# Optimization experiments

Measured on AMD Instinct MI355X. Metric: run time of the kernel, lower is better.

The kernel has to match this reference:

```python
import jax, jax.numpy as jnp
import numpy as np

N_NODES = 50000
IN_CH = 128
OUT_CH = 64
N_EDGES = 800000


def setup_inputs() -> dict:
    key = jax.random.key(0)
    k_x, k_e, k_w, k_b = jax.random.split(key, 4)
    x = jax.random.normal(k_x, (N_NODES, IN_CH), dtype=jnp.float32)
    edge_index = jax.random.randint(k_e, (2, N_EDGES), 0, N_NODES, dtype=jnp.int64)
    # nn.Linear(in, out, bias=False): weight [out, in], applied as x @ W^T
    W = jax.random.normal(k_w, (OUT_CH, IN_CH), dtype=jnp.float32) * (1.0 / np.sqrt(IN_CH))
    bias = jax.random.normal(k_b, (OUT_CH,), dtype=jnp.float32) * 0.02
    return {"x": x, "edge_index": edge_index, "W": W, "bias": bias}


def reference(x, edge_index, W, bias):
    # linear projection (no bias): [N, in] @ [in, out] -> [N, out]
    h = x @ W.T
    src = edge_index[0]
    dst = edge_index[1]
    # gather source node feats per edge: [E, out]
    msgs = h[src]
    # scatter_add into dest nodes: [N, out]
    out = jax.ops.segment_sum(msgs, dst, num_segments=h.shape[0])
    return out + bias
```

## Files before the change

### kernel.cpp

```cpp
#include <hip/hip_runtime.h>

#define IN_CH 128
#define OUT_CH 64
#define TN 64
#define XS_STRIDE 132
#define WS_STRIDE 129

#define PBLOCKS 512
#define NB 800
#define CAPA 8
#define DCAP 32

__device__ __forceinline__ unsigned f2bf(float f) {
    unsigned u = __float_as_uint(f);
    return (u + 0x7FFFu + ((u >> 16) & 1u)) >> 16;
}

__device__ __forceinline__ void fma4(float4& acc, float s, const float4& wv) {
    acc.x += s * wv.x;
    acc.y += s * wv.y;
    acc.z += s * wv.z;
    acc.w += s * wv.w;
}

__global__ __launch_bounds__(256) void k_fusedA(const float* __restrict__ x,
                                                const float* __restrict__ W,
                                                unsigned* __restrict__ h16,
                                                const int* __restrict__ ei,
                                                unsigned* __restrict__ cells,
                                                int* __restrict__ cntA,
                                                uint2* __restrict__ spill,
                                                int* __restrict__ spillCount,
                                                int nNodes, int nEdges, int gemmBlocks) {
    __shared__ float smem[TN * XS_STRIDE + IN_CH * OUT_CH];
    __shared__ int is64s;
    int tid = threadIdx.x;

    if (blockIdx.x >= gemmBlocks) {
        unsigned* lists = (unsigned*)smem;
        int* curs = (int*)smem + NB * CAPA;
        int pblk = blockIdx.x - gemmBlocks;
        for (int i = tid; i < NB; i += 256) curs[i] = 0;
        if (tid == 0) {
            int v = 1;
#pragma unroll
            for (int j = 0; j < 16; ++j)
                if (ei[2 * j + 1] != 0) v = 0;
            is64s = v;
        }
        __syncthreads();
        int is64 = is64s;

        int chunk = (nEdges + PBLOCKS - 1) / PBLOCKS;
        int e0 = pblk * chunk;
        int e1 = min(e0 + chunk, nEdges);
        for (int e = e0 + tid; e < e1; e += 256) {
            int src, dst;
            if (is64) {
                src = ((const int2*)ei)[e].x;
                dst = ((const int2*)ei)[nEdges + e].x;
            } else {
                src = ei[e];
                dst = ei[nEdges + e];
            }
            if ((unsigned)src >= (unsigned)nNodes) src = 0;
            if ((unsigned)dst >= (unsigned)nNodes) dst = 0;
            int bucket = dst >> 6;
            int rank = (bucket < NB) ? atomicAdd(&curs[bucket], 1) : CAPA;
            if (rank < CAPA) {
                lists[bucket * CAPA + rank] = (unsigned)src | ((unsigned)(dst & 63) << 16);
            } else {
                int sp = atomicAdd(spillCount, 1);
                if (sp < nEdges) spill[sp] = make_uint2((unsigned)src, (unsigned)dst);
            }
        }
        __syncthreads();

        size_t base = (size_t)pblk * NB;
        uint4* cells4 = (uint4*)(cells + base * CAPA);
        for (int j = tid; j < NB * CAPA / 4; j += 256)
            cells4[j] = *(const uint4*)(lists + 4 * j);
        for (int i = tid; i < NB; i += 256)
            cntA[base + i] = min(curs[i], CAPA);
        return;
    }

    float* u  = smem;
    float* wt = smem + TN * XS_STRIDE;
    int nodeBase = blockIdx.x * TN;

    {
        const float4* W4 = (const float4*)W;
        for (int i = tid; i < IN_CH * OUT_CH / 4; i += 256) {
            float4 v = W4[i];
            int o = i >> 5;
            int k = (i & 31) * 4;
            float* d = u + o * WS_STRIDE + k;
            d[0] = v.x; d[1] = v.y; d[2] = v.z; d[3] = v.w;
        }
    }
    __syncthreads();
    {
        int o = tid & 63;
        int k0 = (tid >> 6) * 32;
#pragma unroll 8
        for (int k = k0; k < k0 + 32; ++k)
            wt[k * OUT_CH + o] = u[o * WS_STRIDE + k];
    }
    __syncthreads();
    {
        int remRows = nNodes - nodeBase;
        if (remRows > TN) remRows = TN;
        const float4* X4 = (const float4*)(x + (size_t)nodeBase * IN_CH);
        for (int i = tid; i < TN * IN_CH / 4; i += 256) {
            int r = i >> 5;
            int k = (i & 31) * 4;
            float4 v = make_float4(0.f, 0.f, 0.f, 0.f);
            if (r < remRows) v = X4[i];
            *(float4*)(u + r * XS_STRIDE + k) = v;
        }
    }
    __syncthreads();

    int tx = tid & 15;
    int ty = tid >> 4;

    float4 acc[4];
#pragma unroll
    for (int i = 0; i < 4; ++i) acc[i] = make_float4(0.f, 0.f, 0.f, 0.f);

    const float* wcol = wt + tx * 4;
#pragma unroll 4
    for (int k = 0; k < IN_CH; k += 4) {
        float4 w0 = *(const float4*)(wcol + (k + 0) * OUT_CH);
        float4 w1 = *(const float4*)(wcol + (k + 1) * OUT_CH);
        float4 w2 = *(const float4*)(wcol + (k + 2) * OUT_CH);
        float4 w3 = *(const float4*)(wcol + (k + 3) * OUT_CH);
#pragma unroll
        for (int i = 0; i < 4; ++i) {
            float4 a = *(const float4*)(u + (ty * 4 + i) * XS_STRIDE + k);
            fma4(acc[i], a.x, w0);
            fma4(acc[i], a.y, w1);
            fma4(acc[i], a.z, w2);
            fma4(acc[i], a.w, w3);
        }
    }

#pragma unroll
    for (int i = 0; i < 4; ++i) {
        int n = nodeBase + ty * 4 + i;
        if (n < nNodes) {
            uint2 pk;
            pk.x = f2bf(acc[i].x) | (f2bf(acc[i].y) << 16);
            pk.y = f2bf(acc[i].z) | (f2bf(acc[i].w) << 16);
            *(uint2*)(h16 + (size_t)n * 32 + tx * 2) = pk;
        }
    }
}

__global__ __launch_bounds__(1024) void k_fusedB(const unsigned* __restrict__ cells,
                                                 const int* __restrict__ cntA,
                                                 const unsigned* __restrict__ h16,
                                                 const float* __restrict__ bias,
                                                 float* __restrict__ out,
                                                 uint2* __restrict__ spill,
                                                 int* __restrict__ spillCount,
                                                 int nNodes, int nEdges) {
    __shared__ unsigned nl[64 * DCAP];
    __shared__ int nc[64];
    int tid = threadIdx.x;
    int b = blockIdx.x;
    int nodeBase = b * 64;

    if (tid < 64) nc[tid] = 0;
    __syncthreads();

    if (b < NB) {
        for (int blk = tid; blk < PBLOCKS; blk += 1024) {
            int c = cntA[(size_t)blk * NB + b];
            const unsigned* cb = cells + ((size_t)blk * NB + b) * CAPA;
            uint4 w0 = *(const uint4*)(cb + 0);
            uint4 w1 = *(const uint4*)(cb + 4);
            unsigned w[CAPA] = {w0.x, w0.y, w0.z, w0.w, w1.x, w1.y, w1.z, w1.w};
#pragma unroll
            for (int r = 0; r < CAPA; ++r) {
                if (r < c) {
                    unsigned rec = w[r];
                    int sub = (int)(rec >> 16);
                    int rank = atomicAdd(&nc[sub], 1);
                    if (rank < DCAP) {
                        nl[sub * DCAP + rank] = rec & 0xFFFFu;
                    } else {
                        int sp = atomicAdd(spillCount, 1);
                        if (sp < nEdges) spill[sp] = make_uint2(rec & 0xFFFFu, (unsigned)(nodeBase + sub));
                    }
                }
            }
        }
    }
    __syncthreads();

    int lane = tid & 63;
    int wv   = tid >> 6;
    int half = lane >> 5;
    int cp   = lane & 31;
    float2 bv = *(const float2*)(bias + cp * 2);

#pragma unroll
    for (int i = 0; i < 4; ++i) {
        int sub = wv * 4 + i;
        int node = nodeBase + sub;
        if (node >= nNodes) continue;

        int d = nc[sub];
        if (d > DCAP) d = DCAP;
        int jend = (d + 1) & ~1;

        int myslot = (lane < d) ? (int)nl[sub * DCAP + lane] : 0;

        float2 acc = {0.f, 0.f};
        int j = half;
        for (; j + 6 < jend; j += 8) {
            int s0 = __shfl(myslot, j, 64);
            int s1 = __shfl(myslot, j + 2, 64);
            int s2 = __shfl(myslot, j + 4, 64);
            int s3 = __shfl(myslot, j + 6, 64);
            unsigned v0 = h16[(size_t)s0 * 32 + cp];
            unsigned v1 = h16[(size_t)s1 * 32 + cp];
            unsigned v2 = h16[(size_t)s2 * 32 + cp];
            unsigned v3 = h16[(size_t)s3 * 32 + cp];
            if (j + 6 >= d) v3 = 0;
            acc.x += __uint_as_float(v0 << 16);
            acc.y += __uint_as_float(v0 & 0xFFFF0000u);
            acc.x += __uint_as_float(v1 << 16);
            acc.y += __uint_as_float(v1 & 0xFFFF0000u);
            acc.x += __uint_as_float(v2 << 16);
            acc.y += __uint_as_float(v2 & 0xFFFF0000u);
            acc.x += __uint_as_float(v3 << 16);
            acc.y += __uint_as_float(v3 & 0xFFFF0000u);
        }
        for (; j < jend; j += 2) {
            int s = __shfl(myslot, j, 64);
            unsigned v = h16[(size_t)s * 32 + cp];
            if (j >= d) v = 0;
            acc.x += __uint_as_float(v << 16);
            acc.y += __uint_as_float(v & 0xFFFF0000u);
        }

        acc.x += __shfl_down(acc.x, 32, 64);
        acc.y += __shfl_down(acc.y, 32, 64);
        if (half == 0) {
            float2 o;
            o.x = acc.x + bv.x;
            o.y = acc.y + bv.y;
            *(float2*)(out + (size_t)node * OUT_CH + cp * 2) = o;
        }
    }
}

__global__ __launch_bounds__(256) void k_spill(const uint2* __restrict__ spill,
                                               const int* __restrict__ spillCount,
                                               const unsigned* __restrict__ h16,
                                               float* __restrict__ out, int nEdges) {
    int n = *spillCount;
    if (n > nEdges) n = nEdges;
    long long total = (long long)n * 32;
    for (long long t = blockIdx.x * 256 + threadIdx.x; t < total; t += (long long)gridDim.x * 256) {
        int e = (int)(t >> 5);
        int cp = (int)(t & 31);
        uint2 sd = spill[e];
        unsigned v = h16[(size_t)sd.x * 32 + cp];
        float* o = out + (size_t)sd.y * OUT_CH + cp * 2;
        unsafeAtomicAdd(o + 0, __uint_as_float(v << 16));
        unsafeAtomicAdd(o + 1, __uint_as_float(v & 0xFFFF0000u));
    }
}

extern "C" void kernel_launch(void* const* d_in, const int* in_sizes, int n_in,
                              void* d_out, int out_size, void* d_ws, size_t ws_size,
                              hipStream_t stream) {
    const float* x    = (const float*)d_in[0];
    const int*   ei   = (const int*)d_in[1];
    const float* W    = (const float*)d_in[2];
    const float* bias = (const float*)d_in[3];
    float* out = (float*)d_out;

    int nNodes = in_sizes[0] / IN_CH;
    int nEdges = in_sizes[1] / 2;
    int gemmBlocks = (nNodes + TN - 1) / TN;
    int realBuckets = (nNodes + 63) / 64;

    char* p = (char*)d_ws;
    auto alloc = [&](size_t bytes) {
        char* r = p;
        p += (bytes + 255) & ~(size_t)255;
        return r;
    };
    unsigned* h16        = (unsigned*)alloc((size_t)nNodes * 32 * sizeof(unsigned));
    unsigned* cells      = (unsigned*)alloc((size_t)PBLOCKS * NB * CAPA * sizeof(unsigned));
    int*      cntA       = (int*)alloc((size_t)PBLOCKS * NB * sizeof(int));
    uint2*    spill      = (uint2*)alloc((size_t)nEdges * sizeof(uint2));
    int*      spillCount = (int*)alloc(sizeof(int));

    hipMemsetAsync(spillCount, 0, sizeof(int), stream);
    k_fusedA<<<gemmBlocks + PBLOCKS, 256, 0, stream>>>(x, W, h16, ei, cells, cntA,
                                                       spill, spillCount, nNodes, nEdges, gemmBlocks);
    k_fusedB<<<realBuckets, 1024, 0, stream>>>(cells, cntA, h16, bias, out,
                                               spill, spillCount, nNodes, nEdges);
    k_spill<<<64, 256, 0, stream>>>(spill, spillCount, h16, out, nEdges);
}
```

Measured before the change: 138.3 us.

## Pack bucket counts into cell records and interleave partition and GEMM blocks

Removes the separate per-cell count array by storing each cell's count in the top 4 bits of its first record, so the consumer kernel gets the count from the same 32-byte load and skips one scattered read per cell. It also spreads the edge-partition blocks evenly among the GEMM blocks in the grid instead of putting them all at the end, so memory-bound and compute-bound work run on the GPU at the same time. The packing relies on source indices fitting in 16 bits and the count fitting in 4 bits. The consumer now masks the sub-bucket field to 6 bits so the packed count does not corrupt the first record.

```diff
diff --git a/kernel.cpp b/kernel.cpp
--- a/kernel.cpp
+++ b/kernel.cpp
@@ -28,19 +28,22 @@
                                                 unsigned* __restrict__ h16,
                                                 const int* __restrict__ ei,
                                                 unsigned* __restrict__ cells,
-                                                int* __restrict__ cntA,
                                                 uint2* __restrict__ spill,
                                                 int* __restrict__ spillCount,
-                                                int nNodes, int nEdges, int gemmBlocks) {
+                                                int nNodes, int nEdges, int totalBlocks) {
     __shared__ float smem[TN * XS_STRIDE + IN_CH * OUT_CH];
     __shared__ int is64s;
     int tid = threadIdx.x;
 
-    if (blockIdx.x >= gemmBlocks) {
+    int i = blockIdx.x;
+    long long t = (long long)i * PBLOCKS;
+    int pid = (int)(t / totalBlocks);
+    int isPartA = (int)((t + PBLOCKS) / totalBlocks) > pid;
+
+    if (isPartA) {
         unsigned* lists = (unsigned*)smem;
         int* curs = (int*)smem + NB * CAPA;
-        int pblk = blockIdx.x - gemmBlocks;
-        for (int i = tid; i < NB; i += 256) curs[i] = 0;
+        for (int k = tid; k < NB; k += 256) curs[k] = 0;
         if (tid == 0) {
             int v = 1;
 #pragma unroll
@@ -52,7 +55,7 @@
         int is64 = is64s;
 
         int chunk = (nEdges + PBLOCKS - 1) / PBLOCKS;
-        int e0 = pblk * chunk;
+        int e0 = pid * chunk;
         int e1 = min(e0 + chunk, nEdges);
         for (int e = e0 + tid; e < e1; e += 256) {
             int src, dst;
@@ -76,25 +79,30 @@
         }
         __syncthreads();
 
-        size_t base = (size_t)pblk * NB;
+        size_t base = (size_t)pid * NB;
         uint4* cells4 = (uint4*)(cells + base * CAPA);
-        for (int j = tid; j < NB * CAPA / 4; j += 256)
-            cells4[j] = *(const uint4*)(lists + 4 * j);
-        for (int i = tid; i < NB; i += 256)
-            cntA[base + i] = min(curs[i], CAPA);
+        for (int j = tid; j < NB * CAPA / 4; j += 256) {
+            uint4 v = *(const uint4*)(lists + 4 * j);
+            if ((j & 1) == 0) {
+                int cell = j >> 1;
+                v.x = (v.x & 0x0FFFFFFFu) | ((unsigned)min(curs[cell], CAPA) << 28);
+            }
+            cells4[j] = v;
+        }
         return;
     }
 
+    int gid = i - pid;
     float* u  = smem;
     float* wt = smem + TN * XS_STRIDE;
-    int nodeBase = blockIdx.x * TN;
+    int nodeBase = gid * TN;
 
     {
         const float4* W4 = (const float4*)W;
-        for (int i = tid; i < IN_CH * OUT_CH / 4; i += 256) {
-            float4 v = W4[i];
-            int o = i >> 5;
-            int k = (i & 31) * 4;
+        for (int j = tid; j < IN_CH * OUT_CH / 4; j += 256) {
+            float4 v = W4[j];
+            int o = j >> 5;
+            int k = (j & 31) * 4;
             float* d = u + o * WS_STRIDE + k;
             d[0] = v.x; d[1] = v.y; d[2] = v.z; d[3] = v.w;
         }
@@ -112,11 +120,11 @@
         int remRows = nNodes - nodeBase;
         if (remRows > TN) remRows = TN;
         const float4* X4 = (const float4*)(x + (size_t)nodeBase * IN_CH);
-        for (int i = tid; i < TN * IN_CH / 4; i += 256) {
-            int r = i >> 5;
-            int k = (i & 31) * 4;
+        for (int j = tid; j < TN * IN_CH / 4; j += 256) {
+            int r = j >> 5;
+            int k = (j & 31) * 4;
             float4 v = make_float4(0.f, 0.f, 0.f, 0.f);
-            if (r < remRows) v = X4[i];
+            if (r < remRows) v = X4[j];
             *(float4*)(u + r * XS_STRIDE + k) = v;
         }
     }
@@ -127,7 +135,7 @@
 
     float4 acc[4];
 #pragma unroll
-    for (int i = 0; i < 4; ++i) acc[i] = make_float4(0.f, 0.f, 0.f, 0.f);
+    for (int q = 0; q < 4; ++q) acc[q] = make_float4(0.f, 0.f, 0.f, 0.f);
 
     const float* wcol = wt + tx * 4;
 #pragma unroll 4
@@ -137,29 +145,28 @@
         float4 w2 = *(const float4*)(wcol + (k + 2) * OUT_CH);
         float4 w3 = *(const float4*)(wcol + (k + 3) * OUT_CH);
 #pragma unroll
-        for (int i = 0; i < 4; ++i) {
-            float4 a = *(const float4*)(u + (ty * 4 + i) * XS_STRIDE + k);
-            fma4(acc[i], a.x, w0);
-            fma4(acc[i], a.y, w1);
-            fma4(acc[i], a.z, w2);
-            fma4(acc[i], a.w, w3);
-        }
-    }
-
-#pragma unroll
-    for (int i = 0; i < 4; ++i) {
-        int n = nodeBase + ty * 4 + i;
+        for (int q = 0; q < 4; ++q) {
+            float4 a = *(const float4*)(u + (ty * 4 + q) * XS_STRIDE + k);
+            fma4(acc[q], a.x, w0);
+            fma4(acc[q], a.y, w1);
+            fma4(acc[q], a.z, w2);
+            fma4(acc[q], a.w, w3);
+        }
+    }
+
+#pragma unroll
+    for (int q = 0; q < 4; ++q) {
+        int n = nodeBase + ty * 4 + q;
         if (n < nNodes) {
             uint2 pk;
-            pk.x = f2bf(acc[i].x) | (f2bf(acc[i].y) << 16);
-            pk.y = f2bf(acc[i].z) | (f2bf(acc[i].w) << 16);
+            pk.x = f2bf(acc[q].x) | (f2bf(acc[q].y) << 16);
+            pk.y = f2bf(acc[q].z) | (f2bf(acc[q].w) << 16);
             *(uint2*)(h16 + (size_t)n * 32 + tx * 2) = pk;
         }
     }
 }
 
 __global__ __launch_bounds__(1024) void k_fusedB(const unsigned* __restrict__ cells,
-                                                 const int* __restrict__ cntA,
                                                  const unsigned* __restrict__ h16,
                                                  const float* __restrict__ bias,
                                                  float* __restrict__ out,
@@ -177,16 +184,17 @@
 
     if (b < NB) {
         for (int blk = tid; blk < PBLOCKS; blk += 1024) {
-            int c = cntA[(size_t)blk * NB + b];
             const unsigned* cb = cells + ((size_t)blk * NB + b) * CAPA;
             uint4 w0 = *(const uint4*)(cb + 0);
             uint4 w1 = *(const uint4*)(cb + 4);
+            int c = (int)(w0.x >> 28);
+            if (c > CAPA) c = CAPA;
             unsigned w[CAPA] = {w0.x, w0.y, w0.z, w0.w, w1.x, w1.y, w1.z, w1.w};
 #pragma unroll
             for (int r = 0; r < CAPA; ++r) {
                 if (r < c) {
                     unsigned rec = w[r];
-                    int sub = (int)(rec >> 16);
+                    int sub = (int)(rec >> 16) & 63;
                     int rank = atomicAdd(&nc[sub], 1);
                     if (rank < DCAP) {
                         nl[sub * DCAP + rank] = rec & 0xFFFFu;
@@ -207,8 +215,8 @@
     float2 bv = *(const float2*)(bias + cp * 2);
 
 #pragma unroll
-    for (int i = 0; i < 4; ++i) {
-        int sub = wv * 4 + i;
+    for (int q = 0; q < 4; ++q) {
+        int sub = wv * 4 + q;
         int node = nodeBase + sub;
         if (node >= nNodes) continue;
 
@@ -289,6 +297,7 @@
     int nEdges = in_sizes[1] / 2;
     int gemmBlocks = (nNodes + TN - 1) / TN;
     int realBuckets = (nNodes + 63) / 64;
+    int totalBlocks = gemmBlocks + PBLOCKS;
 
     char* p = (char*)d_ws;
     auto alloc = [&](size_t bytes) {
@@ -298,14 +307,13 @@
     };
     unsigned* h16        = (unsigned*)alloc((size_t)nNodes * 32 * sizeof(unsigned));
     unsigned* cells      = (unsigned*)alloc((size_t)PBLOCKS * NB * CAPA * sizeof(unsigned));
-    int*      cntA       = (int*)alloc((size_t)PBLOCKS * NB * sizeof(int));
     uint2*    spill      = (uint2*)alloc((size_t)nEdges * sizeof(uint2));
     int*      spillCount = (int*)alloc(sizeof(int));
 
     hipMemsetAsync(spillCount, 0, sizeof(int), stream);
-    k_fusedA<<<gemmBlocks + PBLOCKS, 256, 0, stream>>>(x, W, h16, ei, cells, cntA,
-                                                       spill, spillCount, nNodes, nEdges, gemmBlocks);
-    k_fusedB<<<realBuckets, 1024, 0, stream>>>(cells, cntA, h16, bias, out,
+    k_fusedA<<<totalBlocks, 256, 0, stream>>>(x, W, h16, ei, cells,
+                                              spill, spillCount, nNodes, nEdges, totalBlocks);
+    k_fusedB<<<realBuckets, 1024, 0, stream>>>(cells, h16, bias, out,
                                                spill, spillCount, nNodes, nEdges);
     k_spill<<<64, 256, 0, stream>>>(spill, spillCount, h16, out, nEdges);
 }
```

Measured after the change: 137.1 us. About the same (-0.9%).
